# Kernel optimization log

Hardware: AMD Instinct MI355X
Metric: run time of the kernel (lower is better)

The kernel has to match this reference:

```python
import jax, jax.numpy as jnp
import numpy as np

B, L, D, DI = 4, 4096, 2048, 256
LN_EPS = 1e-5


def setup_inputs() -> dict:
    key = jax.random.key(0)
    ks = jax.random.split(key, 5)
    x = jax.random.normal(ks[0], (B, L, D), jnp.float32)
    # xavier-ish scale for in/out projections, std=0.01 for scan projections (as in _init_weights)
    W_in = jax.random.normal(ks[1], (D, DI), jnp.float32) * np.float32(1.0 / np.sqrt(D))
    W_fwd = jax.random.normal(ks[2], (DI, 2 * DI), jnp.float32) * np.float32(0.01)
    W_bwd = jax.random.normal(ks[3], (DI, 2 * DI), jnp.float32) * np.float32(0.01)
    W_out = jax.random.normal(ks[4], (2 * DI, D), jnp.float32) * np.float32(1.0 / np.sqrt(2 * DI))
    gamma = jnp.ones((D,), jnp.float32)
    beta = jnp.zeros((D,), jnp.float32)
    return {"x": x, "W_in": W_in, "W_fwd": W_fwd, "W_bwd": W_bwd, "W_out": W_out, "gamma": gamma, "beta": beta}


def _scan_dir(z, Wp):
    """Gated linear recurrence h_t = delta_t * h_{t-1} + gate_t, with delta/gate from one GEMM.
    z: [B, L, d]; Wp: [d, 2d] -> returns [B, L, d]."""
    d = z.shape[-1]
    o = jnp.einsum("bld,de->ble", z, Wp)          # [B, L, 2d]
    delta = jax.nn.sigmoid(o[..., :d])             # [B, L, d]
    gate = o[..., d:] * z                          # [B, L, d]

    def step(h, dg):
        dlt, g = dg
        h = h * dlt + g
        return h, h

    h0 = jnp.zeros_like(z[:, 0])                   # [B, d]
    _, hs = jax.lax.scan(step, h0, (jnp.swapaxes(delta, 0, 1), jnp.swapaxes(gate, 0, 1)))
    return jnp.swapaxes(hs, 0, 1)                  # [B, L, d]


def reference(x, W_in, W_fwd, W_bwd, W_out, gamma, beta):
    z = jnp.einsum("bld,de->ble", x, W_in)         # [B, L, DI]
    h_fwd = _scan_dir(z, W_fwd)
    h_bwd = _scan_dir(z[:, ::-1], W_bwd)[:, ::-1]
    out = jnp.einsum("ble,ed->bld", jnp.concatenate([h_fwd, h_bwd], axis=-1), W_out)
    y = out + x                                    # residual
    mu = jnp.mean(y, axis=-1, keepdims=True)
    var = jnp.var(y, axis=-1, keepdims=True)
    return (y - mu) * jax.lax.rsqrt(var + LN_EPS) * gamma + beta
```

## Files before the change

### kernel.cpp

```cpp
#include <hip/hip_runtime.h>
#include <hip/hip_bf16.h>

using bf16 = __hip_bfloat16;
typedef float float4v __attribute__((ext_vector_type(4)));
typedef __bf16 bf16x8 __attribute__((ext_vector_type(8)));
typedef unsigned short ushort4v __attribute__((ext_vector_type(4)));
typedef unsigned short ushort8v __attribute__((ext_vector_type(8)));

#define B_  4
#define L_  4096
#define D_  2048
#define DI_ 256
#define M_  (B_*L_)
#define NC  64
#define LC  (L_/NC)

__device__ inline float bf2f(bf16 x) { return __bfloat162float(x); }
__device__ inline bf16  f2bf(float x) { return __float2bfloat16(x); }

__device__ inline void store4bf(bf16* p, float4v v) {
    ushort4v u;
#pragma unroll
    for (int i = 0; i < 4; i++) {
        bf16 h = f2bf(v[i]);
        u[i] = *(unsigned short*)&h;
    }
    *(ushort4v*)p = u;
}

__device__ inline float4v load4bf(const bf16* p) {
    ushort4v u = *(const ushort4v*)p;
    float4v v;
#pragma unroll
    for (int i = 0; i < 4; i++) v[i] = __uint_as_float(((unsigned)u[i]) << 16);
    return v;
}

__device__ inline ushort8v cvt8(float4v a, float4v b) {
    ushort8v u;
#pragma unroll
    for (int i = 0; i < 4; i++) {
        bf16 h0 = f2bf(a[i]); u[i]     = *(unsigned short*)&h0;
        bf16 h1 = f2bf(b[i]); u[i + 4] = *(unsigned short*)&h1;
    }
    return u;
}

__device__ __forceinline__ void gload_lds16(const bf16* g, bf16* l) {
    __builtin_amdgcn_global_load_lds((const __attribute__((address_space(1))) void*)(g),
                                     (__attribute__((address_space(3))) void*)(l),
                                     16, 0, 0);
}

template<int N> __device__ __forceinline__ void vmwait() {
    asm volatile("s_waitcnt vmcnt(%0)" :: "n"(N) : "memory");
}
template<int N> __device__ __forceinline__ void vmwait_lgkm0() {
    asm volatile("s_waitcnt vmcnt(%0) lgkmcnt(0)" :: "n"(N) : "memory");
}
__device__ __forceinline__ void bar() {
    asm volatile("" ::: "memory");
    __builtin_amdgcn_s_barrier();
    asm volatile("" ::: "memory");
}

__global__ void transpose_cvt(const float* __restrict__ in, bf16* __restrict__ out,
                              int R, int C, int obase) {
    int idx = blockIdx.x * 256 + threadIdx.x;
    if (idx < R * C) {
        int r = idx / C, c = idx - r * C;
        out[(size_t)(c + obase) * R + r] = f2bf(in[idx]);
    }
}

#define BK 32

template<int TBM, int TBN, int EPI, bool AF32>
__global__ __launch_bounds__(256) void gemm_bt(const void* __restrict__ Av,
                                               const bf16* __restrict__ BT,
                                               int K, int N,
                                               bf16* __restrict__ o0, bf16* __restrict__ o1,
                                               bf16* __restrict__ o2, bf16* __restrict__ o3,
                                               const bf16* __restrict__ auxb,
                                               const float* __restrict__ auxf) {
    constexpr int MI  = TBM / 32, NI = TBN / 32, AP = TBM / 64, BP = TBN / 64;
    constexpr int ASZ = TBM * 32, BSZ = TBN * 32;
    constexpr int TOPW = AF32 ? (2 * AP + BP) : (AP + BP);
    constexpr int MIDW = 2 * AP + 2 * BP;
    __shared__ __align__(16) bf16 As[2 * ASZ];
    __shared__ __align__(16) bf16 Bs[2 * BSZ];
    const int tid  = threadIdx.x;
    const int bm   = blockIdx.x, bn = blockIdx.y;
    const int lane = tid & 63, wave = tid >> 6;
    const int wm   = (wave >> 1) * (TBM / 2), wn = (wave & 1) * (TBN / 2);
    const int l15  = lane & 15, quad = lane >> 4;
    const int rsub  = lane >> 2;
    const int kslot = (lane & 3) ^ ((lane >> 3) & 3);
    const int sq    = quad ^ ((l15 >> 1) & 3);
    const int sr    = tid >> 2, scs = tid & 3;
    const int swslot = scs ^ ((sr >> 1) & 3);

    float4v acc[MI][NI] = {};
    const float* Af = (const float*)Av;
    const bf16*  Ab = (const bf16*)Av;
    float4v fa0[AP][2], fa1[AP][2];

    auto stage_a = [&](int buf, int kk) {
#pragma unroll
        for (int p = 0; p < AP; p++) {
            int rbase = wave * (TBM / 4) + p * 16;
            gload_lds16(Ab + (size_t)(bm * TBM + rbase + rsub) * K + kk + kslot * 8,
                        As + buf * ASZ + rbase * 32 + lane * 8);
        }
    };
    auto stage_b = [&](int buf, int kk) {
#pragma unroll
        for (int p = 0; p < BP; p++) {
            int rbase = wave * (TBN / 4) + p * 16;
            gload_lds16(BT + (size_t)(bn * TBN + rbase + rsub) * K + kk + kslot * 8,
                        Bs + buf * BSZ + rbase * 32 + lane * 8);
        }
    };
    auto load_a_f32 = [&](float4v (&fa)[AP][2], int kk) {
#pragma unroll
        for (int p = 0; p < AP; p++) {
            const float* src = Af + (size_t)(bm * TBM + p * 64 + sr) * K + kk + scs * 8;
            fa[p][0] = *(const float4v*)src;
            fa[p][1] = *(const float4v*)(src + 4);
        }
    };
    auto write_a_f32 = [&](float4v (&fa)[AP][2], int buf) {
#pragma unroll
        for (int p = 0; p < AP; p++)
            *(ushort8v*)(As + buf * ASZ + (p * 64 + sr) * 32 + swslot * 8)
                = cvt8(fa[p][0], fa[p][1]);
    };
    auto compute = [&](int buf) {
        bf16x8 af[MI], bfr[NI];
#pragma unroll
        for (int mi = 0; mi < MI; mi++)
            af[mi] = *(const bf16x8*)(As + buf * ASZ + (wm + mi * 16 + l15) * 32 + sq * 8);
#pragma unroll
        for (int ni = 0; ni < NI; ni++)
            bfr[ni] = *(const bf16x8*)(Bs + buf * BSZ + (wn + ni * 16 + l15) * 32 + sq * 8);
        __builtin_amdgcn_s_setprio(1);
#pragma unroll
        for (int mi = 0; mi < MI; mi++)
#pragma unroll
            for (int ni = 0; ni < NI; ni++)
                acc[mi][ni] = __builtin_amdgcn_mfma_f32_16x16x32_bf16(
                    bfr[ni], af[mi], acc[mi][ni], 0, 0, 0);
        __builtin_amdgcn_s_setprio(0);
    };

    const int nt = K / BK;

    if constexpr (AF32) {
        load_a_f32(fa0, 0);
        stage_b(0, 0);
        load_a_f32(fa1, BK);
        stage_b(1, BK);
        vmwait<MIDW>();
        write_a_f32(fa0, 0);

        auto body = [&](int t, int buf, float4v (&fT)[AP][2], float4v (&fT1)[AP][2]) {
            if (t == nt - 1) vmwait_lgkm0<0>(); else vmwait_lgkm0<TOPW>();
            bar();
            compute(buf);
            bar();
            if (t + 2 < nt) {
                load_a_f32(fT, (t + 2) * BK);
                stage_b(buf, (t + 2) * BK);
                vmwait<MIDW>();
            } else if (t + 1 < nt) {
                vmwait<BP>();
            }
            if (t + 1 < nt) write_a_f32(fT1, buf ^ 1);
        };
        for (int t = 0; t < nt; t += 2) {
            body(t, 0, fa0, fa1);
            body(t + 1, 1, fa1, fa0);
        }
    } else {
        stage_a(0, 0);  stage_b(0, 0);
        stage_a(1, BK); stage_b(1, BK);
        for (int t = 0; t < nt; t++) {
            if (t == nt - 1) vmwait<0>(); else vmwait<TOPW>();
            bar();
            compute(t & 1);
            bar();
            if (t + 2 < nt) {
                stage_a(t & 1, (t + 2) * BK);
                stage_b(t & 1, (t + 2) * BK);
            }
        }
    }

#pragma unroll
    for (int mi = 0; mi < MI; mi++) {
#pragma unroll
        for (int ni = 0; ni < NI; ni++) {
            int row = bm * TBM + wm + mi * 16 + l15;
            int col = bn * TBN + wn + ni * 16 + quad * 4;
            float4v v = acc[mi][ni];
            if (EPI == 0) {
                store4bf(o0 + (size_t)row * N + col, v);
            } else if (EPI == 1) {
                int sel = col >> 8, d = col & 255;
                bf16* dst = (sel == 0) ? o0 : (sel == 1) ? o1 : (sel == 2) ? o2 : o3;
                if (sel & 1) {
                    float4v z4 = load4bf(auxb + (size_t)row * DI_ + d);
#pragma unroll
                    for (int i = 0; i < 4; i++) v[i] *= z4[i];
                } else {
#pragma unroll
                    for (int i = 0; i < 4; i++) v[i] = 1.f / (1.f + __expf(-v[i]));
                }
                store4bf(dst + (size_t)row * DI_ + d, v);
            } else {
                float4v r = *(const float4v*)(auxf + (size_t)row * N + col);
#pragma unroll
                for (int i = 0; i < 4; i++) v[i] += r[i];
                store4bf(o0 + (size_t)row * N + col, v);
            }
        }
    }
}

__global__ __launch_bounds__(256) void scan_agg(const bf16* __restrict__ del_f,
                                                const bf16* __restrict__ gat_f,
                                                const bf16* __restrict__ del_b,
                                                const bf16* __restrict__ gat_b,
                                                float* __restrict__ aggA,
                                                float* __restrict__ aggB) {
    int c = blockIdx.x, b = blockIdx.y, dir = blockIdx.z, d = threadIdx.x;
    const bf16* delta = dir ? del_b : del_f;
    const bf16* gate  = dir ? gat_b : gat_f;
    float Ap = 1.f, h = 0.f;
    for (int i = 0; i < LC; i++) {
        int t = dir ? (L_ - 1 - (c * LC + i)) : (c * LC + i);
        size_t base = ((size_t)(b * L_ + t)) * DI_ + d;
        float dlt = bf2f(delta[base]);
        float g   = bf2f(gate[base]);
        Ap *= dlt;
        h = h * dlt + g;
    }
    size_t idx = (((size_t)dir * B_ + b) * NC + c) * DI_ + d;
    aggA[idx] = Ap;
    aggB[idx] = h;
}

__global__ void scan_mid(const float* __restrict__ aggA, const float* __restrict__ aggB,
                         float* __restrict__ Hin) {
    int b = blockIdx.x, dir = blockIdx.y, d = threadIdx.x;
    float h = 0.f;
    for (int c = 0; c < NC; c++) {
        size_t idx = (((size_t)dir * B_ + b) * NC + c) * DI_ + d;
        Hin[idx] = h;
        h = aggA[idx] * h + aggB[idx];
    }
}

__global__ __launch_bounds__(256) void scan_fix(const bf16* __restrict__ del_f,
                                                const bf16* __restrict__ gat_f,
                                                const bf16* __restrict__ del_b,
                                                const bf16* __restrict__ gat_b,
                                                const float* __restrict__ Hin,
                                                bf16* __restrict__ hcat) {
    int c = blockIdx.x, b = blockIdx.y, dir = blockIdx.z, d = threadIdx.x;
    const bf16* delta = dir ? del_b : del_f;
    const bf16* gate  = dir ? gat_b : gat_f;
    float h = Hin[(((size_t)dir * B_ + b) * NC + c) * DI_ + d];
    int colbase = dir * DI_;
    for (int i = 0; i < LC; i++) {
        int t = dir ? (L_ - 1 - (c * LC + i)) : (c * LC + i);
        size_t base = ((size_t)(b * L_ + t)) * DI_ + d;
        float dlt = bf2f(delta[base]);
        float g   = bf2f(gate[base]);
        h = h * dlt + g;
        hcat[((size_t)(b * L_ + t)) * (2 * DI_) + colbase + d] = f2bf(h);
    }
}

__global__ __launch_bounds__(256) void ln_kernel(const bf16* __restrict__ y,
                                                 const float* __restrict__ gamma,
                                                 const float* __restrict__ beta,
                                                 float* __restrict__ outp) {
    __shared__ float ss[4], ssq[4];
    int row = blockIdx.x, tid = threadIdx.x;
    size_t base = (size_t)row * D_ + tid * 8;
    uint4 raw = *(const uint4*)(y + base);
    const unsigned short* u = (const unsigned short*)&raw;
    float v[8];
    float s = 0.f, sq = 0.f;
#pragma unroll
    for (int i = 0; i < 8; i++) {
        v[i] = __uint_as_float(((unsigned)u[i]) << 16);
        s += v[i];
        sq += v[i] * v[i];
    }
    for (int o = 32; o > 0; o >>= 1) { s += __shfl_down(s, o); sq += __shfl_down(sq, o); }
    if ((tid & 63) == 0) { ss[tid >> 6] = s; ssq[tid >> 6] = sq; }
    __syncthreads();
    float S  = ss[0] + ss[1] + ss[2] + ss[3];
    float SQ = ssq[0] + ssq[1] + ssq[2] + ssq[3];
    float mean = S * (1.f / D_);
    float var  = SQ * (1.f / D_) - mean * mean;
    float rstd = rsqrtf(var + 1e-5f);
    float4v g0 = *(const float4v*)(gamma + tid * 8);
    float4v g1 = *(const float4v*)(gamma + tid * 8 + 4);
    float4v b0 = *(const float4v*)(beta + tid * 8);
    float4v b1 = *(const float4v*)(beta + tid * 8 + 4);
    float4v r0, r1;
#pragma unroll
    for (int i = 0; i < 4; i++) {
        r0[i] = (v[i] - mean) * rstd * g0[i] + b0[i];
        r1[i] = (v[i + 4] - mean) * rstd * g1[i] + b1[i];
    }
    *(float4v*)(outp + base)     = r0;
    *(float4v*)(outp + base + 4) = r1;
}

extern "C" void kernel_launch(void* const* d_in, const int* in_sizes, int n_in,
                              void* d_out, int out_size, void* d_ws, size_t ws_size,
                              hipStream_t stream) {
    (void)in_sizes; (void)n_in; (void)out_size; (void)ws_size;
    const float* x     = (const float*)d_in[0];
    const float* W_in  = (const float*)d_in[1];
    const float* W_fwd = (const float*)d_in[2];
    const float* W_bwd = (const float*)d_in[3];
    const float* W_out = (const float*)d_in[4];
    const float* gamma = (const float*)d_in[5];
    const float* beta  = (const float*)d_in[6];
    float* out = (float*)d_out;

    char* ws = (char*)d_ws;
    size_t off = 0;
    auto alloc = [&](size_t bytes) -> char* {
        char* p = ws + off;
        off += (bytes + 255) & ~(size_t)255;
        return p;
    };
    bf16*  WinT   = (bf16*)alloc((size_t)DI_ * D_ * 2);
    bf16*  WpT    = (bf16*)alloc((size_t)1024 * DI_ * 2);
    bf16*  WoutT  = (bf16*)alloc((size_t)D_ * 2 * DI_ * 2);
    bf16*  z      = (bf16*)alloc((size_t)M_ * DI_ * 2);
    bf16*  del_f  = (bf16*)alloc((size_t)M_ * DI_ * 2);
    bf16*  gat_f  = (bf16*)alloc((size_t)M_ * DI_ * 2);
    bf16*  del_b  = (bf16*)alloc((size_t)M_ * DI_ * 2);
    bf16*  gat_b  = (bf16*)alloc((size_t)M_ * DI_ * 2);
    bf16*  hcat   = (bf16*)alloc((size_t)M_ * 2 * DI_ * 2);
    bf16*  ybuf   = (bf16*)alloc((size_t)M_ * D_ * 2);
    float* aggA   = (float*)alloc((size_t)2 * B_ * NC * DI_ * 4);
    float* aggB   = (float*)alloc((size_t)2 * B_ * NC * DI_ * 4);
    float* Hin    = (float*)alloc((size_t)2 * B_ * NC * DI_ * 4);

    transpose_cvt<<<(D_ * DI_ + 255) / 256, 256, 0, stream>>>(W_in, WinT, D_, DI_, 0);
    transpose_cvt<<<(DI_ * 2 * DI_ + 255) / 256, 256, 0, stream>>>(W_fwd, WpT, DI_, 2 * DI_, 0);
    transpose_cvt<<<(DI_ * 2 * DI_ + 255) / 256, 256, 0, stream>>>(W_bwd, WpT, DI_, 2 * DI_, 2 * DI_);
    transpose_cvt<<<(2 * DI_ * D_ + 255) / 256, 256, 0, stream>>>(W_out, WoutT, 2 * DI_, D_, 0);

    gemm_bt<64, 256, 0, true><<<dim3(M_ / 64, 1), 256, 0, stream>>>(
        x, WinT, D_, DI_, z, nullptr, nullptr, nullptr, nullptr, nullptr);

    gemm_bt<128, 128, 1, false><<<dim3(M_ / 128, 1024 / 128), 256, 0, stream>>>(
        z, WpT, DI_, 1024, del_f, gat_f, del_b, gat_b, z, nullptr);

    scan_agg<<<dim3(NC, B_, 2), DI_, 0, stream>>>(del_f, gat_f, del_b, gat_b, aggA, aggB);
    scan_mid<<<dim3(B_, 2), DI_, 0, stream>>>(aggA, aggB, Hin);
    scan_fix<<<dim3(NC, B_, 2), DI_, 0, stream>>>(del_f, gat_f, del_b, gat_b, Hin, hcat);

    gemm_bt<128, 128, 2, false><<<dim3(M_ / 128, D_ / 128), 256, 0, stream>>>(
        hcat, WoutT, 2 * DI_, D_, ybuf, nullptr, nullptr, nullptr, nullptr, x);

    ln_kernel<<<M_, 256, 0, stream>>>(ybuf, gamma, beta, out);
}
```

Measured before the change: 446.2 us.

## Deepen f32-A GEMM pipeline to three stages, stagger K order, split N tiles

The f32-input GEMM moves from a double-buffered to a triple-buffered pipeline, keeping two K-tiles of global loads in flight, with adjusted vmcnt waits and a loop unrolled by three. Each block now starts its K loop at a different offset derived from its block indices, so concurrent blocks read different columns at the same moment, which is meant to reduce DRAM and channel contention. The first projection GEMM uses 64x128 tiles over a 2-wide N grid instead of 64x256, doubling the block count for occupancy. In exchange x is read twice, there is more LDS and register use, and the rotation assumes nt is a power of two.

```diff
diff --git a/kernel.cpp b/kernel.cpp
--- a/kernel.cpp
+++ b/kernel.cpp
@@ -84,11 +84,11 @@
                                                const bf16* __restrict__ auxb,
                                                const float* __restrict__ auxf) {
     constexpr int MI  = TBM / 32, NI = TBN / 32, AP = TBM / 64, BP = TBN / 64;
+    constexpr int AI  = 2 * AP;
     constexpr int ASZ = TBM * 32, BSZ = TBN * 32;
-    constexpr int TOPW = AF32 ? (2 * AP + BP) : (AP + BP);
-    constexpr int MIDW = 2 * AP + 2 * BP;
-    __shared__ __align__(16) bf16 As[2 * ASZ];
-    __shared__ __align__(16) bf16 Bs[2 * BSZ];
+    constexpr int ND  = AF32 ? 3 : 2;
+    __shared__ __align__(16) bf16 As[ND * ASZ];
+    __shared__ __align__(16) bf16 Bs[ND * BSZ];
     const int tid  = threadIdx.x;
     const int bm   = blockIdx.x, bn = blockIdx.y;
     const int lane = tid & 63, wave = tid >> 6;
@@ -103,7 +103,12 @@
     float4v acc[MI][NI] = {};
     const float* Af = (const float*)Av;
     const bf16*  Ab = (const bf16*)Av;
-    float4v fa0[AP][2], fa1[AP][2];
+    float4v fa0[AP][2], fa1[AP][2], fa2[AP][2];
+
+    const int nt   = K / BK;
+    const int mask = nt - 1;
+    const int t0   = (bm * 5 + bn * 3) & mask;
+    auto T = [&](int i) { return ((i + t0) & mask) * BK; };
 
     auto stage_a = [&](int buf, int kk) {
 #pragma unroll
@@ -153,45 +158,49 @@
         __builtin_amdgcn_s_setprio(0);
     };
 
-    const int nt = K / BK;
-
     if constexpr (AF32) {
-        load_a_f32(fa0, 0);
-        stage_b(0, 0);
-        load_a_f32(fa1, BK);
-        stage_b(1, BK);
-        vmwait<MIDW>();
+        load_a_f32(fa0, T(0)); stage_b(0, T(0));
+        load_a_f32(fa1, T(1)); stage_b(1, T(1));
+        load_a_f32(fa2, T(2)); stage_b(2, T(2));
+        vmwait<2 * AI + 3 * BP>();
         write_a_f32(fa0, 0);
 
-        auto body = [&](int t, int buf, float4v (&fT)[AP][2], float4v (&fT1)[AP][2]) {
-            if (t == nt - 1) vmwait_lgkm0<0>(); else vmwait_lgkm0<TOPW>();
+        auto body = [&](int t, int bi, int nbuf,
+                        float4v (&fcur)[AP][2], float4v (&fnext)[AP][2]) {
+            int k = nt - 1 - t;
+            if (k >= 2)      vmwait_lgkm0<2 * (AI + BP)>();
+            else if (k == 1) vmwait_lgkm0<AI + BP>();
+            else             vmwait_lgkm0<0>();
             bar();
-            compute(buf);
+            compute(bi);
             bar();
-            if (t + 2 < nt) {
-                load_a_f32(fT, (t + 2) * BK);
-                stage_b(buf, (t + 2) * BK);
-                vmwait<MIDW>();
-            } else if (t + 1 < nt) {
-                vmwait<BP>();
+            if (t + 3 < nt) { load_a_f32(fcur, T(t + 3)); stage_b(bi, T(t + 3)); }
+            if (t + 1 < nt) {
+                if (t + 3 < nt)      vmwait<2 * AI + 3 * BP>();
+                else if (t + 2 < nt) vmwait<AI + 2 * BP>();
+                else                 vmwait<BP>();
+                write_a_f32(fnext, nbuf);
             }
-            if (t + 1 < nt) write_a_f32(fT1, buf ^ 1);
         };
-        for (int t = 0; t < nt; t += 2) {
-            body(t, 0, fa0, fa1);
-            body(t + 1, 1, fa1, fa0);
-        }
+        int t = 0;
+        for (; t + 3 <= nt; t += 3) {
+            body(t,     0, 1, fa0, fa1);
+            body(t + 1, 1, 2, fa1, fa2);
+            body(t + 2, 2, 0, fa2, fa0);
+        }
+        if (t < nt)     body(t,     0, 1, fa0, fa1);
+        if (t + 1 < nt) body(t + 1, 1, 2, fa1, fa2);
     } else {
-        stage_a(0, 0);  stage_b(0, 0);
-        stage_a(1, BK); stage_b(1, BK);
+        stage_a(0, T(0)); stage_b(0, T(0));
+        stage_a(1, T(1)); stage_b(1, T(1));
         for (int t = 0; t < nt; t++) {
-            if (t == nt - 1) vmwait<0>(); else vmwait<TOPW>();
+            if (t == nt - 1) vmwait<0>(); else vmwait<AP + BP>();
             bar();
             compute(t & 1);
             bar();
             if (t + 2 < nt) {
-                stage_a(t & 1, (t + 2) * BK);
-                stage_b(t & 1, (t + 2) * BK);
+                stage_a(t & 1, T(t + 2));
+                stage_b(t & 1, T(t + 2));
             }
         }
     }
@@ -360,7 +369,7 @@
     transpose_cvt<<<(DI_ * 2 * DI_ + 255) / 256, 256, 0, stream>>>(W_bwd, WpT, DI_, 2 * DI_, 2 * DI_);
     transpose_cvt<<<(2 * DI_ * D_ + 255) / 256, 256, 0, stream>>>(W_out, WoutT, 2 * DI_, D_, 0);
 
-    gemm_bt<64, 256, 0, true><<<dim3(M_ / 64, 1), 256, 0, stream>>>(
+    gemm_bt<64, 128, 0, true><<<dim3(M_ / 64, 2), 256, 0, stream>>>(
         x, WinT, D_, DI_, z, nullptr, nullptr, nullptr, nullptr, nullptr);
 
     gemm_bt<128, 128, 1, false><<<dim3(M_ / 128, 1024 / 128), 256, 0, stream>>>(
```

Result: faster. 436.8 us (-2.1%).
